# Kernel tuning notes

Measured on AMD Instinct MI355X. Metric: run time of the kernel, lower is better.

The kernel has to match this reference:

```python
import jax, jax.numpy as jnp
import numpy as np

N = 20000      # nodes
E = 320000     # edges (avg degree 16)
F_IN = 14
F_OUT = 9
H = 128        # hidden
L = 6          # message passing layers
ED = 3         # edge_dim
MSG_IN = 2 * H + ED  # 259


def _w(k, shape):
    return jax.random.normal(k, shape, jnp.float32) / np.sqrt(shape[0]).astype(np.float32)


def setup_inputs() -> dict:
    key = jax.random.key(0)
    ks = jax.random.split(key, 16)
    x = jax.random.normal(ks[0], (N, F_IN), jnp.float32)
    edge_index = jax.random.randint(ks[1], (2, E), 0, N, jnp.int64)
    edge_attr = jax.random.normal(ks[2], (E, ED), jnp.float32)
    # encoder: Linear(14,128) -> SiLU -> Linear(128,128)
    enc_w1 = _w(ks[3], (F_IN, H)); enc_b1 = jnp.zeros((H,), jnp.float32)
    enc_w2 = _w(ks[4], (H, H));    enc_b2 = jnp.zeros((H,), jnp.float32)
    # L EdgeConv layers: MLP(259->128) -> SiLU -> (128->128), stacked on leading dim
    kc = jax.random.split(ks[5], 2 * L)
    conv_w1 = jnp.stack([_w(kc[i], (MSG_IN, H)) for i in range(L)])
    conv_b1 = jnp.zeros((L, H), jnp.float32)
    conv_w2 = jnp.stack([_w(kc[L + i], (H, H)) for i in range(L)])
    conv_b2 = jnp.zeros((L, H), jnp.float32)
    # decoder: 128->128 SiLU 128->64 SiLU 64->9
    dec_w1 = _w(ks[6], (H, H));       dec_b1 = jnp.zeros((H,), jnp.float32)
    dec_w2 = _w(ks[7], (H, H // 2));  dec_b2 = jnp.zeros((H // 2,), jnp.float32)
    dec_w3 = _w(ks[8], (H // 2, F_OUT)); dec_b3 = jnp.zeros((F_OUT,), jnp.float32)
    return dict(x=x, edge_index=edge_index, edge_attr=edge_attr,
                enc_w1=enc_w1, enc_b1=enc_b1, enc_w2=enc_w2, enc_b2=enc_b2,
                conv_w1=conv_w1, conv_b1=conv_b1, conv_w2=conv_w2, conv_b2=conv_b2,
                dec_w1=dec_w1, dec_b1=dec_b1, dec_w2=dec_w2, dec_b2=dec_b2,
                dec_w3=dec_w3, dec_b3=dec_b3)


def _mlp2(x, w1, b1, w2, b2):
    return jnp.dot(jax.nn.silu(jnp.dot(x, w1) + b1), w2) + b2


def reference(x, edge_index, edge_attr,
              enc_w1, enc_b1, enc_w2, enc_b2,
              conv_w1, conv_b1, conv_w2, conv_b2,
              dec_w1, dec_b1, dec_w2, dec_b2, dec_w3, dec_b3):
    src, dst = edge_index[0], edge_index[1]
    # in-degree for mean aggregation (computed once; structure is fixed)
    deg = jnp.maximum(
        jax.ops.segment_sum(jnp.ones((E,), jnp.float32), dst, num_segments=N), 1.0)
    h = _mlp2(x, enc_w1, enc_b1, enc_w2, enc_b2)  # (N, H)
    for l in range(L):
        # gather-compute-scatter EdgeConv: msg MLP on [h_dst, h_src, edge_attr]
        m_in = jnp.concatenate([h[dst], h[src], edge_attr], axis=-1)  # (E, 2H+ED)
        m = _mlp2(m_in, conv_w1[l], conv_b1[l], conv_w2[l], conv_b2[l])  # (E, H)
        agg = jax.ops.segment_sum(m, dst, num_segments=N) / deg[:, None]  # (N, H)
        h = h + agg  # residual; dropout is identity in eval mode
    h = jax.nn.silu(jnp.dot(h, dec_w1) + dec_b1)
    h = jax.nn.silu(jnp.dot(h, dec_w2) + dec_b2)
    return jnp.dot(h, dec_w3) + dec_b3  # (N, F_OUT)
```

## Files before the change

### kernel.cpp

```cpp
#include <hip/hip_runtime.h>
#include <hip/hip_bf16.h>

#define NN 20000
#define EE 320000
#define HD 128

typedef _Float16 half8 __attribute__((ext_vector_type(8)));
typedef _Float16 half4 __attribute__((ext_vector_type(4)));
typedef _Float16 half2v __attribute__((ext_vector_type(2)));
typedef float floatx4 __attribute__((ext_vector_type(4)));
typedef float float2v __attribute__((ext_vector_type(2)));

__device__ __forceinline__ float silu_f(float x){
  float e = __expf(-x);
  return x * __builtin_amdgcn_rcpf(1.f + e);
}

__device__ __forceinline__ bool ei_is64(const int* __restrict__ ei){
  return (ei[1] | ei[3] | ei[5] | ei[7]) == 0;
}
__device__ __forceinline__ int ei_src(const int* __restrict__ ei, int e, bool is64){
  return is64 ? ei[2*(size_t)e] : ei[e];
}
__device__ __forceinline__ int ei_dst(const int* __restrict__ ei, int e, bool is64){
  return is64 ? ei[2*(size_t)EE + 2*(size_t)e] : ei[EE + e];
}

__global__ __launch_bounds__(256) void sentinel_kernel(float* __restrict__ out, int n, float val){
  int i = blockIdx.x*256 + threadIdx.x;
  if (i < n) out[i] = val;
}

__global__ __launch_bounds__(256) void pack_all_kernel(const float* __restrict__ cw1,
                                                       const float* __restrict__ cw2,
                                                       const float* __restrict__ dw1,
                                                       const float* __restrict__ dw2,
                                                       _Float16* __restrict__ w1p,
                                                       _Float16* __restrict__ w2p,
                                                       _Float16* __restrict__ w1dp,
                                                       _Float16* __restrict__ w2dp){
  int idx = blockIdx.x*256 + threadIdx.x;
  if (idx < 196608){
    int j   = idx & 7;
    int ln  = (idx >> 3) & 63;
    int rest= idx >> 9;
    int cb  = rest & 15;
    int rest2 = rest >> 4;
    int ks  = rest2 & 3;
    int l   = rest2 >> 2;
    int k = ks*32 + (ln>>4)*8 + j;
    int c = cb*16 + (ln&15);
    float v = (c < 128) ? cw1[(size_t)l*33152 + (size_t)k*128 + c]
                        : cw1[(size_t)l*33152 + (size_t)(128+k)*128 + (c-128)];
    w1p[idx] = (_Float16)v;
  } else if (idx < 294912){
    int t = idx - 196608;
    int j   = t & 7;
    int ln  = (t >> 3) & 63;
    int rest= t >> 9;
    int cb  = rest & 7;
    int rest2 = rest >> 3;
    int ks  = rest2 & 3;
    int l   = rest2 >> 2;
    int k = ks*32 + (ln>>4)*8 + j;
    int c = cb*16 + (ln&15);
    w2p[t] = (_Float16)cw2[(size_t)l*16384 + (size_t)k*128 + c];
  } else {
    int t2 = idx - 294912;
    if (t2 < 16384){
      int j = t2 & 7, ln = (t2>>3)&63, cb = (t2>>9)&7, ks = t2>>12;
      int k = ks*32 + (ln>>4)*8 + j;
      int c = cb*16 + (ln&15);
      w1dp[t2] = (_Float16)dw1[(size_t)k*128 + c];
    } else {
      int t = t2 - 16384;
      int j = t & 7, ln = (t>>3)&63, cb = (t>>9)&3, ks = t>>11;
      int k = ks*32 + (ln>>4)*8 + j;
      int c = cb*16 + (ln&15);
      w2dp[t] = (_Float16)dw2[(size_t)k*64 + c];
    }
  }
}

__global__ __launch_bounds__(256) void count_kernel(const int* __restrict__ ei, int* __restrict__ cnt){
  int e = blockIdx.x*256 + threadIdx.x;
  bool is64 = ei_is64(ei);
  atomicAdd(&cnt[ei_dst(ei, e, is64)], 1);
}

__global__ __launch_bounds__(1024) void scan_kernel(int* __restrict__ cntcur,
                                                    int* __restrict__ row_start,
                                                    float* __restrict__ invd){
  __shared__ int part[1024];
  const int t = threadIdx.x;
  const int base = t*20;
  int loc[20];
  int sum = 0;
  #pragma unroll
  for (int i=0;i<20;++i){
    int n = base+i;
    int v = (n < NN) ? cntcur[n] : 0;
    loc[i] = sum; sum += v;
  }
  part[t] = sum;
  __syncthreads();
  for (int off=1; off<1024; off<<=1){
    int v = (t >= off) ? part[t-off] : 0;
    __syncthreads();
    part[t] += v;
    __syncthreads();
  }
  int pre = (t > 0) ? part[t-1] : 0;
  #pragma unroll
  for (int i=0;i<20;++i){
    int n = base+i;
    if (n < NN){
      int rs = pre + loc[i];
      int deg = ((i<19)?loc[i+1]:sum) - loc[i];
      row_start[n] = rs;
      invd[n] = (deg > 0) ? 1.f/(float)deg : 0.f;
      cntcur[n] = rs;
    }
  }
  if (t == 1023) row_start[NN] = part[1023];
}

__global__ __launch_bounds__(256) void scatter_kernel(const int* __restrict__ ei,
                                                      const float* __restrict__ eattr,
                                                      int* __restrict__ cur,
                                                      int4* __restrict__ rec){
  int e = blockIdx.x*256 + threadIdx.x;
  bool is64 = ei_is64(ei);
  int s = ei_src(ei, e, is64);
  int d = ei_dst(ei, e, is64);
  int pos = atomicAdd(&cur[d], 1);
  int4 r;
  r.x = __float_as_int(eattr[(size_t)e*3+0]);
  r.y = __float_as_int(eattr[(size_t)e*3+1]);
  r.z = __float_as_int(eattr[(size_t)e*3+2]);
  r.w = s*256;
  rec[pos] = r;
}

__global__ __launch_bounds__(128) void encoder_kernel(
    const float* __restrict__ x, const float* __restrict__ w1, const float* __restrict__ b1,
    const float* __restrict__ w2, const float* __restrict__ b2,
    float* __restrict__ h, _Float16* __restrict__ hh)
{
  __shared__ float xs[16][14];
  __shared__ float s1[16][128];
  const int n0 = blockIdx.x*16;
  const int tid = threadIdx.x;
  for (int idx=tid; idx<224; idx+=128){
    int i = idx/14, k = idx%14;
    xs[i][k] = x[(size_t)(n0+i)*14 + k];
  }
  __syncthreads();
  const int o = tid;
  float acc[16];
  float bv = b1[o];
  #pragma unroll
  for (int i=0;i<16;++i) acc[i] = bv;
  for (int k=0;k<14;++k){
    float w = w1[k*128+o];
    #pragma unroll
    for (int i=0;i<16;++i) acc[i] += xs[i][k]*w;
  }
  #pragma unroll
  for (int i=0;i<16;++i) s1[i][o] = silu_f(acc[i]);
  __syncthreads();
  float bv2 = b2[o];
  #pragma unroll
  for (int i=0;i<16;++i) acc[i] = bv2;
  for (int k=0;k<128;k+=4){
    float w0=w2[(k+0)*128+o], w1v=w2[(k+1)*128+o], w2v=w2[(k+2)*128+o], w3v=w2[(k+3)*128+o];
    #pragma unroll
    for (int i=0;i<16;++i){
      float4 sv = *(const float4*)&s1[i][k];
      acc[i] += sv.x*w0 + sv.y*w1v + sv.z*w2v + sv.w*w3v;
    }
  }
  #pragma unroll
  for (int i=0;i<16;++i){
    size_t off = (size_t)(n0+i)*HD + o;
    h[off] = acc[i];
    hh[off] = (_Float16)acc[i];
  }
}

__global__ __launch_bounds__(256) void proj_kernel(
    const _Float16* __restrict__ hh, const _Float16* __restrict__ w1p,
    const float* __restrict__ b1, _Float16* __restrict__ UV)
{
  const int tid = threadIdx.x;
  const int wv  = tid >> 6;
  const int ln  = tid & 63;
  const int q   = ln >> 4;
  const int m   = ln & 15;
  const int n0  = blockIdx.x*16;

  floatx4 acc[4];
  #pragma unroll
  for (int j=0;j<4;++j) acc[j] = (floatx4){0.f,0.f,0.f,0.f};

  #pragma unroll
  for (int ks=0; ks<4; ++ks){
    half8 a = *(const half8*)(hh + (size_t)(n0+m)*HD + ks*32 + q*8);
    const _Float16* wb = w1p + (size_t)(ks*16*64 + ln)*8;
    #pragma unroll
    for (int j=0; j<4; ++j){
      half8 b = *(const half8*)(wb + (size_t)(wv*4+j)*512);
      acc[j] = __builtin_amdgcn_mfma_f32_16x16x32_f16(a, b, acc[j], 0,0,0);
    }
  }
  #pragma unroll
  for (int j=0; j<4; ++j){
    const int c = (wv*4+j)*16 + m;
    const float bias = (c < 128) ? b1[c] : 0.f;
    #pragma unroll
    for (int r=0;r<4;++r)
      UV[(size_t)(n0+q*4+r)*256 + c] = (_Float16)(acc[j][r] + bias);
  }
}

__device__ __forceinline__ float2v edge_contrib(int4 r, half2v v, float2v u,
                                                float2v wc0, float2v wc1, float2v wc2){
  float2v p = u;
  p += __int_as_float(r.x) * wc0;
  p += __int_as_float(r.y) * wc1;
  p += __int_as_float(r.z) * wc2;
  p[0] += (float)v[0];
  p[1] += (float)v[1];
  float2v s;
  s[0] = silu_f(p[0]);
  s[1] = silu_f(p[1]);
  return s;
}

__global__ __launch_bounds__(256) void edge_agg_kernel(
    const _Float16* __restrict__ UV, const int* __restrict__ row_start,
    const int4* __restrict__ rec,
    const float* __restrict__ w1e, const float* __restrict__ invd,
    _Float16* __restrict__ S)
{
  const int tid = threadIdx.x;
  const int wv  = __builtin_amdgcn_readfirstlane(tid >> 6);
  const int ln  = tid & 63;
  const int n   = blockIdx.x*4 + wv;
  const int c0  = ln*2;

  const float2v wc0 = *(const float2v*)(w1e +   0 + c0);
  const float2v wc1 = *(const float2v*)(w1e + 128 + c0);
  const float2v wc2 = *(const float2v*)(w1e + 256 + c0);

  half2v uvp = *(const half2v*)(UV + (size_t)n*256 + c0);
  float2v u; u[0] = (float)uvp[0]; u[1] = (float)uvp[1];

  const int rs = row_start[n], re = row_start[n+1];
  float2v a0 = {0.f,0.f}, a1 = {0.f,0.f}, a2 = {0.f,0.f}, a3 = {0.f,0.f};

  const int nq = (re - rs) >> 2;
  int e = rs;
  for (int q = 0; q < nq; ++q, e += 4){
    const int4 r0 = rec[e+0];
    const int4 r1 = rec[e+1];
    const int4 r2 = rec[e+2];
    const int4 r3 = rec[e+3];
    const half2v v0 = *(const half2v*)(UV + (size_t)r0.w + 128 + c0);
    const half2v v1 = *(const half2v*)(UV + (size_t)r1.w + 128 + c0);
    const half2v v2 = *(const half2v*)(UV + (size_t)r2.w + 128 + c0);
    const half2v v3 = *(const half2v*)(UV + (size_t)r3.w + 128 + c0);
    a0 += edge_contrib(r0, v0, u, wc0, wc1, wc2);
    a1 += edge_contrib(r1, v1, u, wc0, wc1, wc2);
    a2 += edge_contrib(r2, v2, u, wc0, wc1, wc2);
    a3 += edge_contrib(r3, v3, u, wc0, wc1, wc2);
  }
  if (e < re){
    const int e1 = (e+1 < re) ? e+1 : e;
    const int e2 = (e+2 < re) ? e+2 : e;
    const int4 r0 = rec[e];
    const int4 r1 = rec[e1];
    const int4 r2 = rec[e2];
    const half2v v0 = *(const half2v*)(UV + (size_t)r0.w + 128 + c0);
    const half2v v1 = *(const half2v*)(UV + (size_t)r1.w + 128 + c0);
    const half2v v2 = *(const half2v*)(UV + (size_t)r2.w + 128 + c0);
    a0 += edge_contrib(r0, v0, u, wc0, wc1, wc2);
    if (e+1 < re) a1 += edge_contrib(r1, v1, u, wc0, wc1, wc2);
    if (e+2 < re) a2 += edge_contrib(r2, v2, u, wc0, wc1, wc2);
  }
  float2v a = (a0 + a1) + (a2 + a3);
  const float iv = invd[n];
  half2v outv; outv[0] = (_Float16)(a[0]*iv); outv[1] = (_Float16)(a[1]*iv);
  *(half2v*)(S + (size_t)n*HD + c0) = outv;
}

__global__ __launch_bounds__(256) void node_proj_kernel(
    const _Float16* __restrict__ S, const _Float16* __restrict__ w2p,
    const float* __restrict__ b2, const float* __restrict__ invd,
    float* __restrict__ h, _Float16* __restrict__ hh,
    const _Float16* __restrict__ w1pn, const float* __restrict__ b1n,
    _Float16* __restrict__ UV, int do_proj)
{
  __shared__ _Float16 hl[16][136];
  const int tid = threadIdx.x;
  const int wv  = tid >> 6;
  const int ln  = tid & 63;
  const int q   = ln >> 4;
  const int m   = ln & 15;
  const int n0  = blockIdx.x*16;

  floatx4 acc[2];
  acc[0] = (floatx4){0.f,0.f,0.f,0.f};
  acc[1] = (floatx4){0.f,0.f,0.f,0.f};
  #pragma unroll
  for (int ks=0; ks<4; ++ks){
    half8 a = *(const half8*)(S + (size_t)(n0+m)*HD + ks*32 + q*8);
    const _Float16* wb = w2p + (size_t)(ks*8*64 + ln)*8;
    #pragma unroll
    for (int j=0;j<2;++j){
      half8 b = *(const half8*)(wb + (size_t)(wv*2+j)*512);
      acc[j] = __builtin_amdgcn_mfma_f32_16x16x32_f16(a, b, acc[j], 0,0,0);
    }
  }
  float gate[4];
  #pragma unroll
  for (int r=0;r<4;++r) gate[r] = (invd[n0 + q*4 + r] > 0.f) ? 1.f : 0.f;
  #pragma unroll
  for (int j=0; j<2; ++j){
    const int c = (wv*2+j)*16 + m;
    const float bv = b2[c];
    #pragma unroll
    for (int r=0;r<4;++r){
      size_t off = (size_t)(n0+q*4+r)*HD + c;
      float hv = h[off] + acc[j][r] + gate[r]*bv;
      h[off] = hv;
      hh[off] = (_Float16)hv;
      hl[q*4+r][c] = (_Float16)hv;
    }
  }
  __syncthreads();
  if (do_proj){
    floatx4 acc2[4];
    #pragma unroll
    for (int j=0;j<4;++j) acc2[j] = (floatx4){0.f,0.f,0.f,0.f};
    #pragma unroll
    for (int ks=0; ks<4; ++ks){
      half8 a = *(const half8*)&hl[m][ks*32 + q*8];
      const _Float16* wb = w1pn + (size_t)(ks*16*64 + ln)*8;
      #pragma unroll
      for (int j=0; j<4; ++j){
        half8 b = *(const half8*)(wb + (size_t)(wv*4+j)*512);
        acc2[j] = __builtin_amdgcn_mfma_f32_16x16x32_f16(a, b, acc2[j], 0,0,0);
      }
    }
    #pragma unroll
    for (int j=0; j<4; ++j){
      const int c = (wv*4+j)*16 + m;
      const float bias = (c < 128) ? b1n[c] : 0.f;
      #pragma unroll
      for (int r=0;r<4;++r)
        UV[(size_t)(n0+q*4+r)*256 + c] = (_Float16)(acc2[j][r] + bias);
    }
  }
}

__global__ __launch_bounds__(256) void decoder_kernel(
    const _Float16* __restrict__ hh,
    const _Float16* __restrict__ w1dp, const float* __restrict__ db1,
    const _Float16* __restrict__ w2dp, const float* __restrict__ db2,
    const float* __restrict__ dw3, const float* __restrict__ db3,
    float* __restrict__ out)
{
  __shared__ _Float16 d1[16][136];
  __shared__ float s2m[16][66];
  const int tid = threadIdx.x;
  const int wv  = tid >> 6;
  const int ln  = tid & 63;
  const int q   = ln >> 4;
  const int m   = ln & 15;
  const int n0  = blockIdx.x*16;

  floatx4 acc1[2];
  acc1[0] = (floatx4){0.f,0.f,0.f,0.f};
  acc1[1] = (floatx4){0.f,0.f,0.f,0.f};
  #pragma unroll
  for (int ks=0; ks<4; ++ks){
    half8 a = *(const half8*)(hh + (size_t)(n0+m)*HD + ks*32 + q*8);
    const _Float16* wb = w1dp + (size_t)(ks*8*64 + ln)*8;
    #pragma unroll
    for (int j=0; j<2; ++j){
      half8 b = *(const half8*)(wb + (size_t)(wv*2+j)*512);
      acc1[j] = __builtin_amdgcn_mfma_f32_16x16x32_f16(a, b, acc1[j], 0,0,0);
    }
  }
  #pragma unroll
  for (int j=0; j<2; ++j){
    const int c = (wv*2+j)*16 + m;
    const float bv = db1[c];
    #pragma unroll
    for (int r=0;r<4;++r)
      d1[q*4+r][c] = (_Float16)silu_f(acc1[j][r] + bv);
  }
  __syncthreads();

  floatx4 acc2 = (floatx4){0.f,0.f,0.f,0.f};
  #pragma unroll
  for (int ks=0; ks<4; ++ks){
    half8 a = *(const half8*)&d1[m][ks*32 + q*8];
    const _Float16* wb = w2dp + (size_t)(ks*4*64 + ln)*8;
    half8 b = *(const half8*)(wb + (size_t)wv*512);
    acc2 = __builtin_amdgcn_mfma_f32_16x16x32_f16(a, b, acc2, 0,0,0);
  }
  {
    const int c = wv*16 + m;
    const float bv = db2[c];
    #pragma unroll
    for (int r=0;r<4;++r)
      s2m[q*4+r][c] = silu_f(acc2[r] + bv);
  }
  __syncthreads();

  if (tid < 144){
    int i = tid/9, oo = tid%9;
    float a = db3[oo];
    #pragma unroll 8
    for (int k=0;k<64;++k) a += s2m[i][k]*dw3[k*9+oo];
    out[(size_t)(n0+i)*9 + oo] = a;
  }
}

constexpr size_t OFF_H    = 0;
constexpr size_t OFF_HH   = 10240000;
constexpr size_t OFF_UV   = 15360000;
constexpr size_t OFF_S    = 25600000;
constexpr size_t OFF_INVD = 30720000;
constexpr size_t OFF_RS   = 30800000;
constexpr size_t OFF_CUR  = 30880064;
constexpr size_t OFF_REC  = 30960064;
constexpr size_t OFF_W1P  = 36080064;
constexpr size_t OFF_W2P  = 36473280;
constexpr size_t OFF_DW1P = 36669888;
constexpr size_t OFF_DW2P = 36702656;
constexpr size_t WS_NEEDED= 36719040;

extern "C" void kernel_launch(void* const* d_in, const int* in_sizes, int n_in,
                              void* d_out, int out_size, void* d_ws, size_t ws_size,
                              hipStream_t stream)
{
  float* out = (float*)d_out;
  const int nout_blk = (out_size + 255)/256;

  static const int EXP_SIZES[17] = {280000,640000,960000,1792,128,16384,128,
                                    198912,768,98304,768,16384,128,8192,64,576,9};
  if (n_in != 17){
    sentinel_kernel<<<nout_blk, 256, 0, stream>>>(out, out_size, 2.0e7f + (float)n_in*1.0e3f);
    return;
  }
  for (int i = 0; i < 17; ++i){
    if (in_sizes[i] != EXP_SIZES[i]){
      int sz = in_sizes[i] < 99999 ? in_sizes[i] : 99999;
      sentinel_kernel<<<nout_blk, 256, 0, stream>>>(out, out_size,
          1.0e7f + (float)i*1.0e5f + (float)sz);
      return;
    }
  }
  if (ws_size < WS_NEEDED){
    sentinel_kernel<<<nout_blk, 256, 0, stream>>>(out, out_size, 1.0e6f);
    return;
  }

  const float* x       = (const float*)d_in[0];
  const int*   ei      = (const int*)  d_in[1];
  const float* eattr   = (const float*)d_in[2];
  const float* enc_w1  = (const float*)d_in[3];
  const float* enc_b1  = (const float*)d_in[4];
  const float* enc_w2  = (const float*)d_in[5];
  const float* enc_b2  = (const float*)d_in[6];
  const float* conv_w1 = (const float*)d_in[7];
  const float* conv_b1 = (const float*)d_in[8];
  const float* conv_w2 = (const float*)d_in[9];
  const float* conv_b2 = (const float*)d_in[10];
  const float* dec_w1  = (const float*)d_in[11];
  const float* dec_b1  = (const float*)d_in[12];
  const float* dec_w2  = (const float*)d_in[13];
  const float* dec_b2  = (const float*)d_in[14];
  const float* dec_w3  = (const float*)d_in[15];
  const float* dec_b3  = (const float*)d_in[16];

  char* ws = (char*)d_ws;
  float*    h     = (float*)   (ws + OFF_H);
  _Float16* hh    = (_Float16*)(ws + OFF_HH);
  _Float16* UV    = (_Float16*)(ws + OFF_UV);
  _Float16* S     = (_Float16*)(ws + OFF_S);
  float*    invd  = (float*)   (ws + OFF_INVD);
  int*      rstart= (int*)     (ws + OFF_RS);
  int*      cur   = (int*)     (ws + OFF_CUR);
  int4*     rec   = (int4*)    (ws + OFF_REC);
  _Float16* w1p   = (_Float16*)(ws + OFF_W1P);
  _Float16* w2p   = (_Float16*)(ws + OFF_W2P);
  _Float16* w1dp  = (_Float16*)(ws + OFF_DW1P);
  _Float16* w2dp  = (_Float16*)(ws + OFF_DW2P);

  hipMemsetAsync(cur, 0, (size_t)NN*sizeof(int), stream);

  pack_all_kernel<<<1248, 256, 0, stream>>>(conv_w1, conv_w2, dec_w1, dec_w2,
                                            w1p, w2p, w1dp, w2dp);
  count_kernel<<<EE/256, 256, 0, stream>>>(ei, cur);
  scan_kernel<<<1, 1024, 0, stream>>>(cur, rstart, invd);
  scatter_kernel<<<EE/256, 256, 0, stream>>>(ei, eattr, cur, rec);
  encoder_kernel<<<NN/16, 128, 0, stream>>>(x, enc_w1, enc_b1, enc_w2, enc_b2, h, hh);
  proj_kernel<<<NN/16, 256, 0, stream>>>(hh, w1p, conv_b1, UV);
  for (int l=0; l<6; ++l){
    edge_agg_kernel<<<NN/4, 256, 0, stream>>>(UV, rstart, rec,
                                              conv_w1 + (size_t)l*33152 + 32768,
                                              invd, S);
    const int lp = (l < 5) ? l+1 : 0;
    node_proj_kernel<<<NN/16, 256, 0, stream>>>(S, w2p + (size_t)l*16384,
                                                conv_b2 + (size_t)l*128, invd, h, hh,
                                                w1p + (size_t)lp*32768,
                                                conv_b1 + (size_t)lp*128,
                                                UV, (l < 5) ? 1 : 0);
  }
  decoder_kernel<<<NN/16, 256, 0, stream>>>(hh, w1dp, dec_b1, w2dp, dec_b2,
                                            dec_w3, dec_b3, out);
}
```

Measured before the change: 399.1 us.

## Pad CSR rows to multiples of four and split each node across two waves

The CSR build now rounds each node's edge count up to a multiple of four. Padding slots point to a dummy UV row filled with large negative values, so SiLU of those entries is close to zero, and the true degree is kept for the mean. This removes the tail branch in the edge aggregation loop. The edge kernel now gives each node two wavefronts that stride over quad-groups and combine partial sums through shared memory, doubling the block count to raise memory-level parallelism. The cost is an extra fill kernel, larger record and workspace buffers, a block-level sync, and padding edges that do wasted gather work.

```diff
diff --git a/kernel.cpp b/kernel.cpp
--- a/kernel.cpp
+++ b/kernel.cpp
@@ -3,6 +3,7 @@
 
 #define NN 20000
 #define EE 320000
+#define EEP 380000
 #define HD 128
 
 typedef _Float16 half8 __attribute__((ext_vector_type(8)));
@@ -95,12 +96,14 @@
   const int t = threadIdx.x;
   const int base = t*20;
   int loc[20];
+  int truedeg[20];
   int sum = 0;
   #pragma unroll
   for (int i=0;i<20;++i){
     int n = base+i;
     int v = (n < NN) ? cntcur[n] : 0;
-    loc[i] = sum; sum += v;
+    truedeg[i] = v;
+    loc[i] = sum; sum += (v+3)&~3;
   }
   part[t] = sum;
   __syncthreads();
@@ -116,13 +119,27 @@
     int n = base+i;
     if (n < NN){
       int rs = pre + loc[i];
-      int deg = ((i<19)?loc[i+1]:sum) - loc[i];
+      int deg = truedeg[i];
       row_start[n] = rs;
       invd[n] = (deg > 0) ? 1.f/(float)deg : 0.f;
       cntcur[n] = rs;
     }
   }
   if (t == 1023) row_start[NN] = part[1023];
+}
+
+__global__ __launch_bounds__(256) void fill_kernel(int4* __restrict__ rec,
+                                                   _Float16* __restrict__ UV){
+  int i = blockIdx.x*256 + threadIdx.x;
+  if (i < EEP){
+    int4 r; r.x = 0; r.y = 0; r.z = 0; r.w = NN*256;
+    rec[i] = r;
+  }
+  if (blockIdx.x == 0 && threadIdx.x < 64){
+    half4 s;
+    s[0]=s[1]=s[2]=s[3]=(_Float16)(-3000.f);
+    *(half4*)(UV + (size_t)NN*256 + threadIdx.x*4) = s;
+  }
 }
 
 __global__ __launch_bounds__(256) void scatter_kernel(const int* __restrict__ ei,
@@ -237,16 +254,19 @@
   return s;
 }
 
-__global__ __launch_bounds__(256) void edge_agg_kernel(
+__global__ __launch_bounds__(256, 8) void edge_agg_kernel(
     const _Float16* __restrict__ UV, const int* __restrict__ row_start,
     const int4* __restrict__ rec,
     const float* __restrict__ w1e, const float* __restrict__ invd,
     _Float16* __restrict__ S)
 {
+  __shared__ float sAcc[2][64][2];
   const int tid = threadIdx.x;
   const int wv  = __builtin_amdgcn_readfirstlane(tid >> 6);
   const int ln  = tid & 63;
-  const int n   = blockIdx.x*4 + wv;
+  const int nl  = wv >> 1;
+  const int hf  = wv & 1;
+  const int n   = blockIdx.x*2 + nl;
   const int c0  = ln*2;
 
   const float2v wc0 = *(const float2v*)(w1e +   0 + c0);
@@ -257,11 +277,11 @@
   float2v u; u[0] = (float)uvp[0]; u[1] = (float)uvp[1];
 
   const int rs = row_start[n], re = row_start[n+1];
+  const int nq = (re - rs) >> 2;
   float2v a0 = {0.f,0.f}, a1 = {0.f,0.f}, a2 = {0.f,0.f}, a3 = {0.f,0.f};
 
-  const int nq = (re - rs) >> 2;
-  int e = rs;
-  for (int q = 0; q < nq; ++q, e += 4){
+  for (int q = hf; q < nq; q += 2){
+    const int e = rs + q*4;
     const int4 r0 = rec[e+0];
     const int4 r1 = rec[e+1];
     const int4 r2 = rec[e+2];
@@ -275,23 +295,20 @@
     a2 += edge_contrib(r2, v2, u, wc0, wc1, wc2);
     a3 += edge_contrib(r3, v3, u, wc0, wc1, wc2);
   }
-  if (e < re){
-    const int e1 = (e+1 < re) ? e+1 : e;
-    const int e2 = (e+2 < re) ? e+2 : e;
-    const int4 r0 = rec[e];
-    const int4 r1 = rec[e1];
-    const int4 r2 = rec[e2];
-    const half2v v0 = *(const half2v*)(UV + (size_t)r0.w + 128 + c0);
-    const half2v v1 = *(const half2v*)(UV + (size_t)r1.w + 128 + c0);
-    const half2v v2 = *(const half2v*)(UV + (size_t)r2.w + 128 + c0);
-    a0 += edge_contrib(r0, v0, u, wc0, wc1, wc2);
-    if (e+1 < re) a1 += edge_contrib(r1, v1, u, wc0, wc1, wc2);
-    if (e+2 < re) a2 += edge_contrib(r2, v2, u, wc0, wc1, wc2);
-  }
   float2v a = (a0 + a1) + (a2 + a3);
-  const float iv = invd[n];
-  half2v outv; outv[0] = (_Float16)(a[0]*iv); outv[1] = (_Float16)(a[1]*iv);
-  *(half2v*)(S + (size_t)n*HD + c0) = outv;
+
+  if (hf == 1){
+    sAcc[nl][ln][0] = a[0];
+    sAcc[nl][ln][1] = a[1];
+  }
+  __syncthreads();
+  if (hf == 0){
+    a[0] += sAcc[nl][ln][0];
+    a[1] += sAcc[nl][ln][1];
+    const float iv = invd[n];
+    half2v outv; outv[0] = (_Float16)(a[0]*iv); outv[1] = (_Float16)(a[1]*iv);
+    *(half2v*)(S + (size_t)n*HD + c0) = outv;
+  }
 }
 
 __global__ __launch_bounds__(256) void node_proj_kernel(
@@ -432,16 +449,16 @@
 constexpr size_t OFF_H    = 0;
 constexpr size_t OFF_HH   = 10240000;
 constexpr size_t OFF_UV   = 15360000;
-constexpr size_t OFF_S    = 25600000;
-constexpr size_t OFF_INVD = 30720000;
-constexpr size_t OFF_RS   = 30800000;
-constexpr size_t OFF_CUR  = 30880064;
-constexpr size_t OFF_REC  = 30960064;
-constexpr size_t OFF_W1P  = 36080064;
-constexpr size_t OFF_W2P  = 36473280;
-constexpr size_t OFF_DW1P = 36669888;
-constexpr size_t OFF_DW2P = 36702656;
-constexpr size_t WS_NEEDED= 36719040;
+constexpr size_t OFF_S    = 25600512;
+constexpr size_t OFF_INVD = 30720512;
+constexpr size_t OFF_RS   = 30800512;
+constexpr size_t OFF_CUR  = 30880576;
+constexpr size_t OFF_REC  = 30960576;
+constexpr size_t OFF_W1P  = 37040576;
+constexpr size_t OFF_W2P  = 37433792;
+constexpr size_t OFF_DW1P = 37630400;
+constexpr size_t OFF_DW2P = 37663168;
+constexpr size_t WS_NEEDED= 37679552;
 
 extern "C" void kernel_launch(void* const* d_in, const int* in_sizes, int n_in,
                               void* d_out, int out_size, void* d_ws, size_t ws_size,
@@ -505,13 +522,14 @@
 
   pack_all_kernel<<<1248, 256, 0, stream>>>(conv_w1, conv_w2, dec_w1, dec_w2,
                                             w1p, w2p, w1dp, w2dp);
+  fill_kernel<<<(EEP+255)/256, 256, 0, stream>>>(rec, UV);
   count_kernel<<<EE/256, 256, 0, stream>>>(ei, cur);
   scan_kernel<<<1, 1024, 0, stream>>>(cur, rstart, invd);
   scatter_kernel<<<EE/256, 256, 0, stream>>>(ei, eattr, cur, rec);
   encoder_kernel<<<NN/16, 128, 0, stream>>>(x, enc_w1, enc_b1, enc_w2, enc_b2, h, hh);
   proj_kernel<<<NN/16, 256, 0, stream>>>(hh, w1p, conv_b1, UV);
   for (int l=0; l<6; ++l){
-    edge_agg_kernel<<<NN/4, 256, 0, stream>>>(UV, rstart, rec,
+    edge_agg_kernel<<<NN/2, 256, 0, stream>>>(UV, rstart, rec,
                                               conv_w1 + (size_t)l*33152 + 32768,
                                               invd, S);
     const int lp = (l < 5) ? l+1 : 0;
```

Result: slower. 419.0 us (+5.0%).
